# Optimization experiments

Hardware: AMD Instinct MI355X
Metric: run time of the kernel (lower is better)

## Reference

```python
import jax, jax.numpy as jnp
import numpy as np

B, S, D = 4, 4096, 1024
H, DH, F = 16, 64, 64
DFF = 4096
EPS_LN = 1e-5
EPS_ATTN = 1e-6


def setup_inputs() -> dict:
    key = jax.random.key(0)
    ks = jax.random.split(key, 12)
    s = 1.0 / np.sqrt(D)
    inp = {
        'x': jax.random.normal(ks[0], (B, S, D), dtype=jnp.float32),
        'ln1_g': jnp.ones((D,), jnp.float32),
        'ln1_b': jnp.zeros((D,), jnp.float32),
        'wq': jax.random.normal(ks[1], (D, H * DH), jnp.float32) * s,
        'wk': jax.random.normal(ks[2], (D, H * DH), jnp.float32) * s,
        'wv': jax.random.normal(ks[3], (D, H * DH), jnp.float32) * s,
        'proj': jax.random.normal(ks[4], (DH, F), jnp.float32) / np.sqrt(F),
        'wo': jax.random.normal(ks[5], (H * DH, D), jnp.float32) * s,
        'bo': jnp.zeros((D,), jnp.float32),
        'ln2_g': jnp.ones((D,), jnp.float32),
        'ln2_b': jnp.zeros((D,), jnp.float32),
        'w1': jax.random.normal(ks[6], (D, DFF), jnp.float32) * s,
        'b1': jnp.zeros((DFF,), jnp.float32),
        'w2': jax.random.normal(ks[7], (DFF, D), jnp.float32) / np.sqrt(DFF),
        'b2': jnp.zeros((D,), jnp.float32),
    }
    return inp


def _layernorm(x, g, b):
    mu = jnp.mean(x, axis=-1, keepdims=True)
    var = jnp.mean(jnp.square(x - mu), axis=-1, keepdims=True)
    return (x - mu) * jax.lax.rsqrt(var + EPS_LN) * g + b


def _heads(t):  # [B,S,H*DH] -> [B,H,S,DH]
    return t.reshape(B, S, H, DH).transpose(0, 2, 1, 3)


def _feature_map(t, proj):  # [B,H,S,DH] -> [B,H,S,F]
    return jax.nn.relu(jnp.einsum('bhnd,df->bhnf', t, proj)) + EPS_ATTN


def reference(x, ln1_g, ln1_b, wq, wk, wv, proj, wo, bo, ln2_g, ln2_b, w1, b1, w2, b2):
    h = _layernorm(x, ln1_g, ln1_b)
    q = _feature_map(_heads(h @ wq), proj)
    k = _feature_map(_heads(h @ wk), proj)
    v = _heads(h @ wv)
    kv = jnp.einsum('bhnf,bhnd->bhfd', k, v)          # [B,H,F,DH]
    k_sum = k.sum(axis=-2)                            # [B,H,F]
    num = jnp.einsum('bhnf,bhfd->bhnd', q, kv)        # [B,H,S,DH]
    den = jnp.einsum('bhnf,bhf->bhn', q, k_sum) + EPS_ATTN
    attn = num / den[..., None]
    attn = attn.transpose(0, 2, 1, 3).reshape(B, S, H * DH)
    x = x + attn @ wo + bo
    h2 = _layernorm(x, ln2_g, ln2_b)
    ffn = jax.nn.gelu(h2 @ w1 + b1, approximate=False) @ w2 + b2
    return x + ffn
```

## Files before the change

### kernel.cpp

```cpp
#include <hip/hip_runtime.h>
#include <hip/hip_bf16.h>
#include <math.h>

using bf16 = __hip_bfloat16;
typedef __attribute__((ext_vector_type(8))) short short8;
typedef __attribute__((ext_vector_type(4))) float f32x4;

constexpr int Bc = 4, Sc = 4096, Dc = 1024, Hc = 16, DHc = 64, Fc = 64, DFFc = 4096;
constexpr float EPS_LN_C = 1e-5f, EPS_ATTN_C = 1e-6f;
constexpr int KVSPLIT = 16;

static __device__ __forceinline__ float b2f(bf16 v) { return __bfloat162float(v); }
static __device__ __forceinline__ bf16 f2b(float f) { return __float2bfloat16(f); }

__device__ float block_reduce_sum(float v) {
  __shared__ float red[4];
  int lane = threadIdx.x & 63, wid = threadIdx.x >> 6;
#pragma unroll
  for (int off = 32; off > 0; off >>= 1) v += __shfl_down(v, off, 64);
  __syncthreads();
  if (lane == 0) red[wid] = v;
  __syncthreads();
  return red[0] + red[1] + red[2] + red[3];
}

__global__ void ln_kernel(const float* __restrict__ x, const float* __restrict__ g,
                          const float* __restrict__ bta, bf16* __restrict__ out) {
  int row = blockIdx.x;
  const float* xr = x + (size_t)row * Dc;
  int t = threadIdx.x;
  float v[4];
#pragma unroll
  for (int i = 0; i < 4; ++i) v[i] = xr[t + 256 * i];
  float s = block_reduce_sum(v[0] + v[1] + v[2] + v[3]);
  float mu = s * (1.f / Dc);
  float vs = 0.f;
#pragma unroll
  for (int i = 0; i < 4; ++i) { float d = v[i] - mu; vs += d * d; }
  vs = block_reduce_sum(vs);
  float rstd = rsqrtf(vs * (1.f / Dc) + EPS_LN_C);
  bf16* orow = out + (size_t)row * Dc;
#pragma unroll
  for (int i = 0; i < 4; ++i) {
    int c = t + 256 * i;
    orow[c] = f2b((v[i] - mu) * rstd * g[c] + bta[c]);
  }
}

__global__ void tcvt_kernel(const float* __restrict__ in, bf16* __restrict__ out,
                            int K, int N) {
  __shared__ float t[32][33];
  int n0 = blockIdx.x * 32, k0 = blockIdx.y * 32;
  int tid = threadIdx.x;
#pragma unroll
  for (int i = 0; i < 4; ++i) {
    int idx = tid + 256 * i;
    int r = idx >> 5, c = idx & 31;
    t[r][c] = in[(size_t)(k0 + r) * N + n0 + c];
  }
  __syncthreads();
#pragma unroll
  for (int i = 0; i < 4; ++i) {
    int idx = tid + 256 * i;
    int r = idx >> 5, c = idx & 31;
    out[(size_t)(n0 + r) * K + k0 + c] = f2b(t[c][r]);
  }
}


template <int MH, int NH, bool LOADA>
static __device__ __forceinline__ void phase_mfma(
    const ushort* __restrict__ ab, const ushort* __restrict__ bb,
    int wr, int wc, int mrow, int cs0, int cs1,
    short8 af[4][2], f32x4 acc[8][4]) {
  if (LOADA) {
#pragma unroll
    for (int i2 = 0; i2 < 4; ++i2) {
      const ushort* p = ab + (wr * 128 + MH * 64 + i2 * 16 + mrow) * 64;
      af[i2][0] = *(const short8*)(p + cs0);
      af[i2][1] = *(const short8*)(p + cs1);
    }
  }
  short8 bf2[2][2];
#pragma unroll
  for (int j2 = 0; j2 < 2; ++j2) {
    const ushort* p = bb + (wc * 64 + NH * 32 + j2 * 16 + mrow) * 64;
    bf2[j2][0] = *(const short8*)(p + cs0);
    bf2[j2][1] = *(const short8*)(p + cs1);
  }
  __builtin_amdgcn_s_barrier();
  asm volatile("s_waitcnt lgkmcnt(0)");
  __builtin_amdgcn_s_setprio(1);
#pragma unroll
  for (int i2 = 0; i2 < 4; ++i2)
#pragma unroll
    for (int j2 = 0; j2 < 2; ++j2) {
      acc[MH * 4 + i2][NH * 2 + j2] = __builtin_amdgcn_mfma_f32_16x16x32_bf16(
          af[i2][0], bf2[j2][0], acc[MH * 4 + i2][NH * 2 + j2], 0, 0, 0);
      acc[MH * 4 + i2][NH * 2 + j2] = __builtin_amdgcn_mfma_f32_16x16x32_bf16(
          af[i2][1], bf2[j2][1], acc[MH * 4 + i2][NH * 2 + j2], 0, 0, 0);
    }
  __builtin_amdgcn_s_setprio(0);
}

template <int EPI>
__global__ __launch_bounds__(512, 2)
void mgemm256_kernel(const ushort* __restrict__ A, const ushort* __restrict__ Bt,
                     const float* __restrict__ bias, const float* __restrict__ res,
                     float* __restrict__ outF, bf16* __restrict__ outB,
                     int M, int N, int K, int lda, int ldbt) {
  __shared__ ushort As[2][256 * 64];
  __shared__ ushort Bs[2][256 * 64];
  const int tid = threadIdx.x;
  const int wave = tid >> 6, lane = tid & 63;
  const int wr = wave >> 2, wc = wave & 3;
  const int mrow = lane & 15, quad = lane >> 4;

  int nn = gridDim.x, nm = gridDim.y;
  int bid = blockIdx.y * nn + blockIdx.x;
  int mtile, ntile;
  if ((nm & 7) == 0) {
    int xcd = bid & 7, s = bid >> 3;
    int mpx = nm >> 3;
    int mloc = s / nn;
    ntile = s - mloc * nn;
    mtile = xcd * mpx + mloc;
  } else { mtile = blockIdx.y; ntile = blockIdx.x; }
  const int row0 = mtile * 256, col0 = ntile * 256;

  const int srow = tid >> 3;
  const int scol = ((((tid & 7) * 16) ^ ((srow & 7) << 4)) >> 1);
  const ushort* aSrc[4];
  const ushort* bSrc[4];
#pragma unroll
  for (int l = 0; l < 4; ++l) {
    aSrc[l] = A + (size_t)(row0 + l * 64 + srow) * lda + scol;
    bSrc[l] = Bt + (size_t)(col0 + l * 64 + srow) * ldbt + scol;
  }
  const int dstoff = tid * 8;

  auto stage = [&](int kt, int b) {
    const int ko = kt * 64;
#pragma unroll
    for (int l = 0; l < 4; ++l)
      __builtin_amdgcn_global_load_lds(
          (const __attribute__((address_space(1))) void*)(aSrc[l] + ko),
          (__attribute__((address_space(3))) void*)(&As[b][l * 4096 + dstoff]), 16, 0, 0);
#pragma unroll
    for (int l = 0; l < 4; ++l)
      __builtin_amdgcn_global_load_lds(
          (const __attribute__((address_space(1))) void*)(bSrc[l] + ko),
          (__attribute__((address_space(3))) void*)(&Bs[b][l * 4096 + dstoff]), 16, 0, 0);
  };

  const int cs0 = (quad * 8) ^ ((mrow & 7) << 3);
  const int cs1 = (quad * 8 + 32) ^ ((mrow & 7) << 3);

  f32x4 acc[8][4] = {};
  short8 af[4][2];

  stage(0, 0);
  __syncthreads();

  const int NI = K >> 7;
  for (int it = 0; it < NI; ++it) {
    stage(2 * it + 1, 1);
    phase_mfma<0, 0, true >(As[0], Bs[0], wr, wc, mrow, cs0, cs1, af, acc);
    __builtin_amdgcn_s_barrier();
    phase_mfma<0, 1, false>(As[0], Bs[0], wr, wc, mrow, cs0, cs1, af, acc);
    __builtin_amdgcn_s_barrier();
    phase_mfma<1, 0, true >(As[0], Bs[0], wr, wc, mrow, cs0, cs1, af, acc);
    __builtin_amdgcn_s_barrier();
    phase_mfma<1, 1, false>(As[0], Bs[0], wr, wc, mrow, cs0, cs1, af, acc);
    asm volatile("s_waitcnt vmcnt(0)" ::: "memory");
    __builtin_amdgcn_s_barrier();
    if (it + 1 < NI) stage(2 * it + 2, 0);
    phase_mfma<0, 0, true >(As[1], Bs[1], wr, wc, mrow, cs0, cs1, af, acc);
    __builtin_amdgcn_s_barrier();
    phase_mfma<0, 1, false>(As[1], Bs[1], wr, wc, mrow, cs0, cs1, af, acc);
    __builtin_amdgcn_s_barrier();
    phase_mfma<1, 0, true >(As[1], Bs[1], wr, wc, mrow, cs0, cs1, af, acc);
    __builtin_amdgcn_s_barrier();
    phase_mfma<1, 1, false>(As[1], Bs[1], wr, wc, mrow, cs0, cs1, af, acc);
    asm volatile("s_waitcnt vmcnt(0)" ::: "memory");
    __builtin_amdgcn_s_barrier();
  }

#pragma unroll
  for (int i = 0; i < 8; ++i) {
#pragma unroll
    for (int j = 0; j < 4; ++j) {
      int rb = row0 + wr * 128 + i * 16 + quad * 4;
      int c = col0 + wc * 64 + j * 16 + mrow;
#pragma unroll
      for (int r = 0; r < 4; ++r) {
        int rr = rb + r;
        float v = acc[i][j][r];
        if (EPI == 1 || EPI == 2) v += bias[c];
        if (EPI == 3) { if (bias) v += bias[c]; }
        if (EPI == 2) v = 0.5f * v * (1.f + erff(v * 0.70710678118654752f));
        if (EPI == 1 || EPI == 3) v += res[(size_t)rr * N + c];
        if (EPI == 4) {
          outB[((size_t)(c >> 10) * (size_t)(Bc * Sc) + rr) * 1024 + (c & 1023)] = f2b(v);
        } else if (EPI == 0 || EPI == 2) {
          outB[(size_t)rr * N + c] = f2b(v);
        } else {
          outF[(size_t)rr * N + c] = v;
        }
      }
    }
  }
}

__global__ __launch_bounds__(256, 2)
void fm_mfma(const ushort* __restrict__ qin, const ushort* __restrict__ pjt,
             bf16* __restrict__ qf) {
  __shared__ ushort As[256 * 64];
  __shared__ ushort Bs[64 * 64];
  int t = threadIdx.x;
  int wave = t >> 6, lane = t & 63;
  int mrow = lane & 15, quad = lane >> 4;
  int b = blockIdx.z, h = blockIdx.y, s0 = blockIdx.x * 256;
  const ushort* abase = qin + ((size_t)b * Sc + s0) * (Hc * DHc) + h * DHc;

#pragma unroll
  for (int i = 0; i < 8; ++i) {
    int c = t + 256 * i;
    int row = c >> 3, col = (c & 7) * 8;
    __builtin_amdgcn_global_load_lds(
        (const __attribute__((address_space(1))) void*)(abase + (size_t)row * (Hc * DHc) + col),
        (__attribute__((address_space(3))) void*)(As + c * 8), 16, 0, 0);
  }
#pragma unroll
  for (int i = 0; i < 2; ++i) {
    int c = t + 256 * i;
    __builtin_amdgcn_global_load_lds(
        (const __attribute__((address_space(1))) void*)(pjt + c * 8),
        (__attribute__((address_space(3))) void*)(Bs + c * 8), 16, 0, 0);
  }
  __syncthreads();

  f32x4 acc[4][4] = {};
#pragma unroll
  for (int step = 0; step < 2; ++step) {
    short8 af[4], bfv[4];
#pragma unroll
    for (int i = 0; i < 4; ++i)
      af[i] = *(const short8*)(As + (wave * 64 + i * 16 + mrow) * 64 + quad * 8 + step * 32);
#pragma unroll
    for (int j = 0; j < 4; ++j)
      bfv[j] = *(const short8*)(Bs + (j * 16 + mrow) * 64 + quad * 8 + step * 32);
#pragma unroll
    for (int i = 0; i < 4; ++i)
#pragma unroll
      for (int j = 0; j < 4; ++j)
        acc[i][j] = __builtin_amdgcn_mfma_f32_16x16x32_bf16(af[i], bfv[j], acc[i][j], 0, 0, 0);
  }

  size_t obase = ((size_t)(b * Hc + h)) * Sc + s0;
#pragma unroll
  for (int i = 0; i < 4; ++i) {
#pragma unroll
    for (int j = 0; j < 4; ++j) {
      int f = j * 16 + mrow;
#pragma unroll
      for (int r = 0; r < 4; ++r) {
        int s = wave * 64 + i * 16 + quad * 4 + r;
        float v = fmaxf(acc[i][j][r], 0.f) + EPS_ATTN_C;
        qf[(obase + s) * Fc + f] = f2b(v);
      }
    }
  }
}

__global__ __launch_bounds__(256, 2)
void kvp_mfma(const ushort* __restrict__ kf, const ushort* __restrict__ v,
              float* __restrict__ kvp, float* __restrict__ ksump) {
  constexpr int LT = 72;
  __shared__ ushort kfT[64 * LT];
  __shared__ ushort vT[64 * LT];
  int t = threadIdx.x;
  int wave = t >> 6, lane = t & 63;
  int mrow = lane & 15, quad = lane >> 4;
  int split = blockIdx.x, bh = blockIdx.y;
  int b = bh >> 4, h = bh & 15;
  int sbase = split * (Sc / KVSPLIT);

  short8 ones, zero;
#pragma unroll
  for (int i = 0; i < 8; ++i) { ones[i] = (short)0x3F80; zero[i] = 0; }
  short8 bks = (mrow == 0) ? ones : zero;

  f32x4 acc[4] = {};
  f32x4 accks = {};

  for (int sc = 0; sc < Sc / KVSPLIT; sc += 64) {
    __syncthreads();
    int sl = t >> 2, c8 = (t & 3) * 8;
    const ushort* kp = kf + (((size_t)bh * Sc) + sbase + sc + sl) * Fc + c8;
    const ushort* vp = v + (((size_t)b * Sc) + sbase + sc + sl) * (Hc * DHc) + h * DHc + c8;
#pragma unroll
    for (int half = 0; half < 2; ++half) {
      short8 kv8 = *(const short8*)(kp + half * 32);
      short8 vv8 = *(const short8*)(vp + half * 32);
#pragma unroll
      for (int jj = 0; jj < 8; ++jj) {
        kfT[(c8 + half * 32 + jj) * LT + sl] = (ushort)kv8[jj];
        vT[(c8 + half * 32 + jj) * LT + sl] = (ushort)vv8[jj];
      }
    }
    __syncthreads();
#pragma unroll
    for (int step = 0; step < 2; ++step) {
      short8 af = *(const short8*)(kfT + (wave * 16 + mrow) * LT + quad * 8 + step * 32);
      short8 bfv[4];
#pragma unroll
      for (int j = 0; j < 4; ++j)
        bfv[j] = *(const short8*)(vT + (j * 16 + mrow) * LT + quad * 8 + step * 32);
#pragma unroll
      for (int j = 0; j < 4; ++j)
        acc[j] = __builtin_amdgcn_mfma_f32_16x16x32_bf16(af, bfv[j], acc[j], 0, 0, 0);
      accks = __builtin_amdgcn_mfma_f32_16x16x32_bf16(af, bks, accks, 0, 0, 0);
    }
  }

  size_t pbase = (size_t)bh * KVSPLIT + split;
#pragma unroll
  for (int j = 0; j < 4; ++j) {
    int d = j * 16 + mrow;
#pragma unroll
    for (int r = 0; r < 4; ++r) {
      int f = wave * 16 + quad * 4 + r;
      kvp[(pbase * 64 + f) * 64 + d] = acc[j][r];
    }
  }
  if (mrow == 0) {
#pragma unroll
    for (int r = 0; r < 4; ++r) {
      int f = wave * 16 + quad * 4 + r;
      ksump[pbase * 64 + f] = accks[r];
    }
  }
}

__global__ void kvr_kernel(const float* __restrict__ kvp, const float* __restrict__ ksump,
                           bf16* __restrict__ kvt, bf16* __restrict__ ksum16) {
  int bh = blockIdx.x;
  int t = threadIdx.x;
#pragma unroll
  for (int i = 0; i < 16; ++i) {
    int idx = t + 256 * i;
    int f = idx >> 6, d = idx & 63;
    float s = 0.f;
#pragma unroll
    for (int j = 0; j < KVSPLIT; ++j)
      s += kvp[((size_t)bh * KVSPLIT + j) * 4096 + idx];
    kvt[((size_t)bh * 64 + d) * 64 + f] = f2b(s);
  }
  if (t < 64) {
    float s = 0.f;
#pragma unroll
    for (int j = 0; j < KVSPLIT; ++j)
      s += ksump[((size_t)bh * KVSPLIT + j) * 64 + t];
    ksum16[bh * 64 + t] = f2b(s);
  }
}

__global__ __launch_bounds__(256, 2)
void attn_mfma(const ushort* __restrict__ qf, const ushort* __restrict__ kvt,
               const ushort* __restrict__ ksum16, bf16* __restrict__ attn) {
  __shared__ ushort As[256 * 64];
  __shared__ ushort Bs[64 * 64];
  int t = threadIdx.x;
  int wave = t >> 6, lane = t & 63;
  int mrow = lane & 15, quad = lane >> 4;
  int b = blockIdx.z, h = blockIdx.y, s0 = blockIdx.x * 256;
  int bh = b * Hc + h;
  const ushort* abase = qf + (((size_t)bh * Sc) + s0) * Fc;
  const ushort* bbase = kvt + (size_t)bh * 4096;

#pragma unroll
  for (int i = 0; i < 8; ++i) {
    int c = t + 256 * i;
    __builtin_amdgcn_global_load_lds(
        (const __attribute__((address_space(1))) void*)(abase + c * 8),
        (__attribute__((address_space(3))) void*)(As + c * 8), 16, 0, 0);
  }
#pragma unroll
  for (int i = 0; i < 2; ++i) {
    int c = t + 256 * i;
    __builtin_amdgcn_global_load_lds(
        (const __attribute__((address_space(1))) void*)(bbase + c * 8),
        (__attribute__((address_space(3))) void*)(Bs + c * 8), 16, 0, 0);
  }
  short8 zero;
#pragma unroll
  for (int i = 0; i < 8; ++i) zero[i] = 0;
  short8 ksf[2];
#pragma unroll
  for (int step = 0; step < 2; ++step) {
    short8 kv8 = *(const short8*)(ksum16 + bh * 64 + quad * 8 + step * 32);
    ksf[step] = (mrow == 0) ? kv8 : zero;
  }
  __syncthreads();

  f32x4 acc[4][4] = {};
  f32x4 accd[4] = {};
#pragma unroll
  for (int step = 0; step < 2; ++step) {
    short8 af[4], bfv[4];
#pragma unroll
    for (int i = 0; i < 4; ++i)
      af[i] = *(const short8*)(As + (wave * 64 + i * 16 + mrow) * 64 + quad * 8 + step * 32);
#pragma unroll
    for (int j = 0; j < 4; ++j)
      bfv[j] = *(const short8*)(Bs + (j * 16 + mrow) * 64 + quad * 8 + step * 32);
#pragma unroll
    for (int i = 0; i < 4; ++i) {
#pragma unroll
      for (int j = 0; j < 4; ++j)
        acc[i][j] = __builtin_amdgcn_mfma_f32_16x16x32_bf16(af[i], bfv[j], acc[i][j], 0, 0, 0);
      accd[i] = __builtin_amdgcn_mfma_f32_16x16x32_bf16(af[i], ksf[step], accd[i], 0, 0, 0);
    }
  }

#pragma unroll
  for (int i = 0; i < 4; ++i) {
    float inv[4];
#pragma unroll
    for (int r = 0; r < 4; ++r) {
      float den = __shfl(accd[i][r], lane & 48);
      inv[r] = 1.0f / (den + EPS_ATTN_C);
    }
#pragma unroll
    for (int j = 0; j < 4; ++j) {
      int d = j * 16 + mrow;
#pragma unroll
      for (int r = 0; r < 4; ++r) {
        int s = s0 + wave * 64 + i * 16 + quad * 4 + r;
        attn[((size_t)(b * Sc + s)) * (Hc * DHc) + h * DHc + d] = f2b(acc[i][j][r] * inv[r]);
      }
    }
  }
}

extern "C" void kernel_launch(void* const* d_in, const int* in_sizes, int n_in,
                              void* d_out, int out_size, void* d_ws, size_t ws_size,
                              hipStream_t stream) {
  const float* x     = (const float*)d_in[0];
  const float* ln1_g = (const float*)d_in[1];
  const float* ln1_b = (const float*)d_in[2];
  const float* wq    = (const float*)d_in[3];
  const float* wk    = (const float*)d_in[4];
  const float* wv    = (const float*)d_in[5];
  const float* proj  = (const float*)d_in[6];
  const float* wo    = (const float*)d_in[7];
  const float* bo    = (const float*)d_in[8];
  const float* ln2_g = (const float*)d_in[9];
  const float* ln2_b = (const float*)d_in[10];
  const float* w1    = (const float*)d_in[11];
  const float* b1    = (const float*)d_in[12];
  const float* w2    = (const float*)d_in[13];
  const float* b2    = (const float*)d_in[14];
  float* out = (float*)d_out;
  (void)ws_size; (void)in_sizes; (void)n_in; (void)out_size;

  const size_t TOK = (size_t)Bc * Sc;
  const size_t REG = TOK * Dc * sizeof(bf16);
  char* ws = (char*)d_ws;
  bf16* R0 = (bf16*)(ws + 0 * REG);
  bf16* R1 = (bf16*)(ws + 1 * REG);
  bf16* R2 = (bf16*)(ws + 2 * REG);
  bf16* R3 = (bf16*)(ws + 3 * REG);
  bf16* mid = R1;
  float* kvpart = (float*)R2;
  float* kspart = (float*)((char*)R2 + (size_t)64 * KVSPLIT * 4096 * 4);
  char* p = ws + 4 * REG;
  bf16* kvt   = (bf16*)p;                 p += (size_t)64 * 64 * 64 * 2;
  bf16* ksb16 = (bf16*)p;                 p += (size_t)64 * 64 * 2;
  bf16* pjt   = (bf16*)p;                 p += (size_t)64 * 64 * 2;
  bf16* wqt = (bf16*)p;                   p += (size_t)Dc * Dc * 2;
  bf16* wkt = (bf16*)p;                   p += (size_t)Dc * Dc * 2;
  bf16* wvt = (bf16*)p;                   p += (size_t)Dc * Dc * 2;
  bf16* wot = (bf16*)p;                   p += (size_t)Dc * Dc * 2;
  bf16* w1t = (bf16*)p;                   p += (size_t)Dc * DFFc * 2;
  bf16* w2t = (bf16*)p;                   p += (size_t)Dc * DFFc * 2;

  dim3 blk(256);
  dim3 blk512(512);
  tcvt_kernel<<<dim3(Dc / 32, Dc / 32), blk, 0, stream>>>(wq, wqt, Dc, Dc);
  tcvt_kernel<<<dim3(Dc / 32, Dc / 32), blk, 0, stream>>>(wk, wkt, Dc, Dc);
  tcvt_kernel<<<dim3(Dc / 32, Dc / 32), blk, 0, stream>>>(wv, wvt, Dc, Dc);
  tcvt_kernel<<<dim3(Dc / 32, Dc / 32), blk, 0, stream>>>(wo, wot, Dc, Dc);
  tcvt_kernel<<<dim3(DFFc / 32, Dc / 32), blk, 0, stream>>>(w1, w1t, Dc, DFFc);
  tcvt_kernel<<<dim3(Dc / 32, DFFc / 32), blk, 0, stream>>>(w2, w2t, DFFc, Dc);
  tcvt_kernel<<<dim3(2, 2), blk, 0, stream>>>(proj, pjt, 64, 64);

  ln_kernel<<<dim3(TOK), blk, 0, stream>>>(x, ln1_g, ln1_b, R0);

  dim3 gQKV(3072 / 256, TOK / 256);
  mgemm256_kernel<4><<<gQKV, blk512, 0, stream>>>((const ushort*)R0, (const ushort*)wqt,
                                                  nullptr, nullptr, nullptr, R1,
                                                  TOK, 3072, Dc, Dc, Dc);

  dim3 gF(Sc / 256, Hc, Bc);
  fm_mfma<<<gF, blk, 0, stream>>>((const ushort*)R1, (const ushort*)pjt, R0);
  fm_mfma<<<gF, blk, 0, stream>>>((const ushort*)R2, (const ushort*)pjt, R1);

  kvp_mfma<<<dim3(KVSPLIT, Bc * Hc), blk, 0, stream>>>((const ushort*)R1, (const ushort*)R3,
                                                       kvpart, kspart);
  kvr_kernel<<<dim3(Bc * Hc), blk, 0, stream>>>(kvpart, kspart, kvt, ksb16);

  attn_mfma<<<gF, blk, 0, stream>>>((const ushort*)R0, (const ushort*)kvt,
                                    (const ushort*)ksb16, R2);

  dim3 gD(Dc / 256, TOK / 256);
  mgemm256_kernel<1><<<gD, blk512, 0, stream>>>((const ushort*)R2, (const ushort*)wot, bo, x,
                                                out, nullptr, TOK, Dc, Dc, Dc, Dc);

  ln_kernel<<<dim3(TOK), blk, 0, stream>>>(out, ln2_g, ln2_b, R0);

  dim3 gW1(2048 / 256, TOK / 256);
  mgemm256_kernel<2><<<gW1, blk512, 0, stream>>>((const ushort*)R0, (const ushort*)w1t, b1, nullptr,
                                                 nullptr, mid, TOK, 2048, Dc, Dc, Dc);
  mgemm256_kernel<3><<<gD, blk512, 0, stream>>>((const ushort*)mid, (const ushort*)w2t, b2, out,
                                                out, nullptr, TOK, Dc, 2048, 2048, DFFc);
  mgemm256_kernel<2><<<gW1, blk512, 0, stream>>>((const ushort*)R0, (const ushort*)(w1t + (size_t)2048 * Dc), b1 + 2048,
                                                 nullptr, nullptr, mid, TOK, 2048, Dc, Dc, Dc);
  mgemm256_kernel<3><<<gD, blk512, 0, stream>>>((const ushort*)mid, (const ushort*)(w2t + 2048), nullptr, out,
                                                out, nullptr, TOK, Dc, 2048, 2048, DFFc);
}
```

Baseline: 1.030 ms.

## Restructure GEMM mainloop into 4-slot ring with K=32 stages and deeper prefetch

```diff
diff --git a/kernel.cpp b/kernel.cpp
--- a/kernel.cpp
+++ b/kernel.cpp
@@ -68,49 +68,15 @@
 }
 
 
-template <int MH, int NH, bool LOADA>
-static __device__ __forceinline__ void phase_mfma(
-    const ushort* __restrict__ ab, const ushort* __restrict__ bb,
-    int wr, int wc, int mrow, int cs0, int cs1,
-    short8 af[4][2], f32x4 acc[8][4]) {
-  if (LOADA) {
-#pragma unroll
-    for (int i2 = 0; i2 < 4; ++i2) {
-      const ushort* p = ab + (wr * 128 + MH * 64 + i2 * 16 + mrow) * 64;
-      af[i2][0] = *(const short8*)(p + cs0);
-      af[i2][1] = *(const short8*)(p + cs1);
-    }
-  }
-  short8 bf2[2][2];
-#pragma unroll
-  for (int j2 = 0; j2 < 2; ++j2) {
-    const ushort* p = bb + (wc * 64 + NH * 32 + j2 * 16 + mrow) * 64;
-    bf2[j2][0] = *(const short8*)(p + cs0);
-    bf2[j2][1] = *(const short8*)(p + cs1);
-  }
-  __builtin_amdgcn_s_barrier();
-  asm volatile("s_waitcnt lgkmcnt(0)");
-  __builtin_amdgcn_s_setprio(1);
-#pragma unroll
-  for (int i2 = 0; i2 < 4; ++i2)
-#pragma unroll
-    for (int j2 = 0; j2 < 2; ++j2) {
-      acc[MH * 4 + i2][NH * 2 + j2] = __builtin_amdgcn_mfma_f32_16x16x32_bf16(
-          af[i2][0], bf2[j2][0], acc[MH * 4 + i2][NH * 2 + j2], 0, 0, 0);
-      acc[MH * 4 + i2][NH * 2 + j2] = __builtin_amdgcn_mfma_f32_16x16x32_bf16(
-          af[i2][1], bf2[j2][1], acc[MH * 4 + i2][NH * 2 + j2], 0, 0, 0);
-    }
-  __builtin_amdgcn_s_setprio(0);
-}
-
 template <int EPI>
 __global__ __launch_bounds__(512, 2)
 void mgemm256_kernel(const ushort* __restrict__ A, const ushort* __restrict__ Bt,
                      const float* __restrict__ bias, const float* __restrict__ res,
                      float* __restrict__ outF, bf16* __restrict__ outB,
                      int M, int N, int K, int lda, int ldbt) {
-  __shared__ ushort As[2][256 * 64];
-  __shared__ ushort Bs[2][256 * 64];
+  constexpr int SLOT = 256 * 32;
+  __shared__ ushort AsR[4][SLOT];
+  __shared__ ushort BsR[4][SLOT];
   const int tid = threadIdx.x;
   const int wave = tid >> 6, lane = tid & 63;
   const int wr = wave >> 2, wc = wave & 3;
@@ -128,61 +94,76 @@
   } else { mtile = blockIdx.y; ntile = blockIdx.x; }
   const int row0 = mtile * 256, col0 = ntile * 256;
 
-  const int srow = tid >> 3;
-  const int scol = ((((tid & 7) * 16) ^ ((srow & 7) << 4)) >> 1);
-  const ushort* aSrc[4];
-  const ushort* bSrc[4];
-#pragma unroll
-  for (int l = 0; l < 4; ++l) {
-    aSrc[l] = A + (size_t)(row0 + l * 64 + srow) * lda + scol;
-    bSrc[l] = Bt + (size_t)(col0 + l * 64 + srow) * ldbt + scol;
-  }
-  const int dstoff = tid * 8;
-
-  auto stage = [&](int kt, int b) {
-    const int ko = kt * 64;
-#pragma unroll
-    for (int l = 0; l < 4; ++l)
-      __builtin_amdgcn_global_load_lds(
-          (const __attribute__((address_space(1))) void*)(aSrc[l] + ko),
-          (__attribute__((address_space(3))) void*)(&As[b][l * 4096 + dstoff]), 16, 0, 0);
-#pragma unroll
-    for (int l = 0; l < 4; ++l)
-      __builtin_amdgcn_global_load_lds(
-          (const __attribute__((address_space(1))) void*)(bSrc[l] + ko),
-          (__attribute__((address_space(3))) void*)(&Bs[b][l * 4096 + dstoff]), 16, 0, 0);
+  const int srowL = tid >> 2;
+  const int sOff = (((tid & 3) ^ ((tid >> 3) & 3)) << 3);
+  const ushort* aB = A + (size_t)(row0 + srowL) * lda + sOff;
+  const ushort* bB = Bt + (size_t)(col0 + srowL) * ldbt + sOff;
+  const int dst = tid * 8;
+
+  auto stage = [&](int sg, int l) {
+    const int sl = sg & 3;
+    __builtin_amdgcn_global_load_lds(
+        (const __attribute__((address_space(1))) void*)(aB + (size_t)(l * 128) * lda + sg * 32),
+        (__attribute__((address_space(3))) void*)(&AsR[sl][l * 4096 + dst]), 16, 0, 0);
+    __builtin_amdgcn_global_load_lds(
+        (const __attribute__((address_space(1))) void*)(bB + (size_t)(l * 128) * ldbt + sg * 32),
+        (__attribute__((address_space(3))) void*)(&BsR[sl][l * 4096 + dst]), 16, 0, 0);
   };
 
-  const int cs0 = (quad * 8) ^ ((mrow & 7) << 3);
-  const int cs1 = (quad * 8 + 32) ^ ((mrow & 7) << 3);
+  const int cq = (quad << 3) ^ (((mrow >> 1) & 3) << 3);
 
   f32x4 acc[8][4] = {};
-  short8 af[4][2];
-
-  stage(0, 0);
-  __syncthreads();
-
-  const int NI = K >> 7;
-  for (int it = 0; it < NI; ++it) {
-    stage(2 * it + 1, 1);
-    phase_mfma<0, 0, true >(As[0], Bs[0], wr, wc, mrow, cs0, cs1, af, acc);
+  const int NS = K >> 5;
+
+  stage(0, 0); stage(0, 1); stage(1, 0); stage(1, 1); stage(2, 0); stage(2, 1);
+  asm volatile("s_waitcnt vmcnt(8)" ::: "memory");
+  __builtin_amdgcn_s_barrier();
+
+  for (int sg = 0; sg < NS; ++sg) {
+    const ushort* As_ = &AsR[sg & 3][0];
+    const ushort* Bs_ = &BsR[sg & 3][0];
+    short8 afv[4], bfv[4];
+#pragma unroll
+    for (int i2 = 0; i2 < 4; ++i2)
+      afv[i2] = *(const short8*)(As_ + (wr * 128 + i2 * 16 + mrow) * 32 + cq);
+#pragma unroll
+    for (int n = 0; n < 4; ++n)
+      bfv[n] = *(const short8*)(Bs_ + (wc * 64 + (n >> 1) * 32 + (n & 1) * 16 + mrow) * 32 + cq);
+    if (sg + 3 < NS) stage(sg + 3, 0);
+    __builtin_amdgcn_sched_barrier(0);
     __builtin_amdgcn_s_barrier();
-    phase_mfma<0, 1, false>(As[0], Bs[0], wr, wc, mrow, cs0, cs1, af, acc);
+    asm volatile("s_waitcnt lgkmcnt(0)" ::: "memory");
+    __builtin_amdgcn_sched_barrier(0);
+    __builtin_amdgcn_s_setprio(1);
+#pragma unroll
+    for (int i2 = 0; i2 < 4; ++i2)
+#pragma unroll
+      for (int n = 0; n < 4; ++n)
+        acc[i2][n] = __builtin_amdgcn_mfma_f32_16x16x32_bf16(afv[i2], bfv[n], acc[i2][n], 0, 0, 0);
+    __builtin_amdgcn_s_setprio(0);
+    __builtin_amdgcn_sched_barrier(0);
     __builtin_amdgcn_s_barrier();
-    phase_mfma<1, 0, true >(As[0], Bs[0], wr, wc, mrow, cs0, cs1, af, acc);
+#pragma unroll
+    for (int i2 = 0; i2 < 4; ++i2)
+      afv[i2] = *(const short8*)(As_ + (wr * 128 + 64 + i2 * 16 + mrow) * 32 + cq);
+    if (sg + 3 < NS) stage(sg + 3, 1);
+    __builtin_amdgcn_sched_barrier(0);
     __builtin_amdgcn_s_barrier();
-    phase_mfma<1, 1, false>(As[0], Bs[0], wr, wc, mrow, cs0, cs1, af, acc);
-    asm volatile("s_waitcnt vmcnt(0)" ::: "memory");
-    __builtin_amdgcn_s_barrier();
-    if (it + 1 < NI) stage(2 * it + 2, 0);
-    phase_mfma<0, 0, true >(As[1], Bs[1], wr, wc, mrow, cs0, cs1, af, acc);
-    __builtin_amdgcn_s_barrier();
-    phase_mfma<0, 1, false>(As[1], Bs[1], wr, wc, mrow, cs0, cs1, af, acc);
-    __builtin_amdgcn_s_barrier();
-    phase_mfma<1, 0, true >(As[1], Bs[1], wr, wc, mrow, cs0, cs1, af, acc);
-    __builtin_amdgcn_s_barrier();
-    phase_mfma<1, 1, false>(As[1], Bs[1], wr, wc, mrow, cs0, cs1, af, acc);
-    asm volatile("s_waitcnt vmcnt(0)" ::: "memory");
+    asm volatile("s_waitcnt lgkmcnt(0)" ::: "memory");
+    __builtin_amdgcn_sched_barrier(0);
+    __builtin_amdgcn_s_setprio(1);
+#pragma unroll
+    for (int i2 = 0; i2 < 4; ++i2)
+#pragma unroll
+      for (int n = 0; n < 4; ++n)
+        acc[4 + i2][n] = __builtin_amdgcn_mfma_f32_16x16x32_bf16(afv[i2], bfv[n], acc[4 + i2][n], 0, 0, 0);
+    __builtin_amdgcn_s_setprio(0);
+    if (sg + 1 < NS) {
+      if (sg + 3 < NS)      asm volatile("s_waitcnt vmcnt(8)" ::: "memory");
+      else if (sg + 2 < NS) asm volatile("s_waitcnt vmcnt(4)" ::: "memory");
+      else                  asm volatile("s_waitcnt vmcnt(0)" ::: "memory");
+    }
+    __builtin_amdgcn_sched_barrier(0);
     __builtin_amdgcn_s_barrier();
   }
 
```

Result: faster. 885.5 us (-14.0%).
